# Kernel optimization log

Hardware: AMD Instinct MI355X
Metric: run time of the kernel (lower is better)

Reference implementation:

```python
import jax, jax.numpy as jnp
import numpy as np

N_HEADS = 4
NS_STEPS = 5
NS_EPS = 1e-7

def newtonschulz5(G):
    # G: [out, in]; quintic Newton-Schulz, 5 steps. out==in here so no transpose branch needed,
    # but keep the static-shape check for faithfulness.
    a, b, c = 3.4445, -4.775, 2.0315
    X = G / (jnp.linalg.norm(G) + NS_EPS)
    transposed = G.shape[0] > G.shape[1]
    if transposed:
        X = X.T
    def step(X, _):
        A = X @ X.T
        B = b * A + c * (A @ A)
        return a * X + B @ X, None
    X, _ = jax.lax.scan(step, X, None, length=NS_STEPS)
    if transposed:
        X = X.T
    return X

def setup_inputs() -> dict:
    key = jax.random.key(0)
    k1, k2, k3, k4, k5 = jax.random.split(key, 5)
    B, S, D_in, D_out, r = 4, 2048, 4096, 4096, 16
    init_std = 0.01 / np.sqrt(D_out * r)
    return {
        "x": jax.random.normal(k1, (B, S, D_in), dtype=jnp.float32),
        "W": jax.random.normal(k2, (D_out, D_in), dtype=jnp.float32) * 0.02,
        "bias": jax.random.normal(k3, (D_out,), dtype=jnp.float32) * 0.02,
        "lora_A": jax.random.normal(k4, (r, D_in), dtype=jnp.float32),
        "lora_B": jax.random.normal(k5, (D_out, r), dtype=jnp.float32) * init_std,
    }

def reference(x, W, bias, lora_A, lora_B):
    # base linear (frozen weights); dropout is identity (p=0 / eval)
    base_out = jnp.einsum('bsi,oi->bso', x, W) + bias
    r, D_in = lora_A.shape
    D_out = lora_B.shape[0]
    hr = r // N_HEADS
    Ah = lora_A.reshape(N_HEADS, hr, D_in)                       # [h, hr, in]
    Bh = lora_B.reshape(D_out, N_HEADS, hr).transpose(1, 0, 2)    # [h, out, hr]
    G = jnp.einsum('hor,hri->hoi', Bh, Ah)                        # [h, out, in]
    alpha = jnp.sqrt(jnp.sum(G * G, axis=(1, 2)))                 # per-head Frobenius norm
    M = jax.vmap(newtonschulz5)(G)                                # [h, out, in]
    lora_out = jnp.einsum('h,hoi,bsi->bso', alpha, M, x)
    return base_out + lora_out
```

## Files before the change

kernel.cpp:

```cpp
#include <hip/hip_runtime.h>
#include <math.h>

#define MDIM 8192
#define NDIM 4096
#define KDIM 4096

typedef __attribute__((ext_vector_type(8))) _Float16 h8;
typedef __attribute__((ext_vector_type(4))) _Float16 h4;
typedef __attribute__((ext_vector_type(4))) float f32x4;

typedef const __attribute__((address_space(1))) void* gas_ptr;
typedef __attribute__((address_space(3))) void* las_ptr;

__device__ inline void load16_to_lds(const void* g, void* l) {
  __builtin_amdgcn_global_load_lds((gas_ptr)g, (las_ptr)l, 16, 0, 0);
}

__device__ inline void mm4(const double* A, const double* B, double* C) {
#pragma unroll
  for (int p = 0; p < 4; ++p)
#pragma unroll
    for (int q = 0; q < 4; ++q) {
      double s = 0.0;
#pragma unroll
      for (int r = 0; r < 4; ++r) s += A[p * 4 + r] * B[r * 4 + q];
      C[p * 4 + q] = s;
    }
}
__device__ inline void mm4_bt(const double* A, const double* B, double* C) {
#pragma unroll
  for (int p = 0; p < 4; ++p)
#pragma unroll
    for (int q = 0; q < 4; ++q) {
      double s = 0.0;
#pragma unroll
      for (int r = 0; r < 4; ++r) s += A[p * 4 + r] * B[q * 4 + r];
      C[p * 4 + q] = s;
    }
}

__global__ void ns_kernel(const float* __restrict__ lora_A,
                          const float* __restrict__ lora_B,
                          float* __restrict__ E) {
  const int h = blockIdx.x;
  const int tid = threadIdx.x;
  const int lane = tid & 63;
  const int wave = tid >> 6;

  float gu[16], gv[16];
#pragma unroll
  for (int e = 0; e < 16; ++e) { gu[e] = 0.f; gv[e] = 0.f; }

  for (int o = tid; o < NDIM; o += 256) {
    const float4 bv = *(const float4*)(lora_B + (size_t)o * 16 + h * 4);
    const float bb[4] = {bv.x, bv.y, bv.z, bv.w};
#pragma unroll
    for (int p = 0; p < 4; ++p)
#pragma unroll
      for (int q = 0; q < 4; ++q) gu[p * 4 + q] += bb[p] * bb[q];
  }
  for (int i = tid; i < KDIM; i += 256) {
    float aa[4];
#pragma unroll
    for (int p = 0; p < 4; ++p) aa[p] = lora_A[(size_t)(h * 4 + p) * KDIM + i];
#pragma unroll
    for (int p = 0; p < 4; ++p)
#pragma unroll
      for (int q = 0; q < 4; ++q) gv[p * 4 + q] += aa[p] * aa[q];
  }

#pragma unroll
  for (int e = 0; e < 16; ++e) {
#pragma unroll
    for (int off = 32; off > 0; off >>= 1) {
      gu[e] += __shfl_down(gu[e], off, 64);
      gv[e] += __shfl_down(gv[e], off, 64);
    }
  }
  __shared__ float pu[4][16], pv[4][16];
  if (lane == 0) {
#pragma unroll
    for (int e = 0; e < 16; ++e) { pu[wave][e] = gu[e]; pv[wave][e] = gv[e]; }
  }
  __syncthreads();

  if (tid == 0) {
    double gud[16], gvd[16];
#pragma unroll
    for (int e = 0; e < 16; ++e) {
      gud[e] = (double)pu[0][e] + pu[1][e] + pu[2][e] + pu[3][e];
      gvd[e] = (double)pv[0][e] + pv[1][e] + pv[2][e] + pv[3][e];
    }
    double tr = 0.0;
#pragma unroll
    for (int e = 0; e < 16; ++e) tr += gud[e] * gvd[e];
    const double alpha = sqrt(tr);
    const double n0 = alpha + 1e-7;

    double C[16] = {0};
    C[0] = C[5] = C[10] = C[15] = 1.0 / n0;

    const double a = 3.4445, b = -4.775, c = 2.0315;
    for (int it = 0; it < 5; ++it) {
      double T1[16], D[16], DG[16], DGD[16], GuC[16], F[16], Cn[16];
      mm4(C, gvd, T1);
      mm4_bt(T1, C, D);
      mm4(D, gud, DG);
      mm4(DG, D, DGD);
      mm4(gud, C, GuC);
#pragma unroll
      for (int e = 0; e < 16; ++e) F[e] = b * D[e] + c * DGD[e];
      mm4(F, GuC, Cn);
#pragma unroll
      for (int e = 0; e < 16; ++e) C[e] = a * C[e] + Cn[e];
    }
#pragma unroll
    for (int e = 0; e < 16; ++e) E[h * 16 + e] = (float)(alpha * C[e]);
  }
}

__global__ void prep_kernel(const float* __restrict__ x,
                            const float* __restrict__ W,
                            const float* __restrict__ lora_A,
                            const float* __restrict__ lora_B,
                            const float* __restrict__ E,
                            _Float16* __restrict__ Wh,
                            _Float16* __restrict__ Xh) {
  const int tid = threadIdx.x;
  if (blockIdx.x < NDIM) {
    const int o = blockIdx.x;
    __shared__ float coef[16];
    if (tid < 16) {
      const int h = tid >> 2, q = tid & 3;
      float s = 0.f;
#pragma unroll
      for (int p = 0; p < 4; ++p)
        s += lora_B[(size_t)o * 16 + h * 4 + p] * E[h * 16 + p * 4 + q];
      coef[tid] = s;
    }
    __syncthreads();
    float cf[16];
#pragma unroll
    for (int k = 0; k < 16; ++k) cf[k] = coef[k];

    for (int i = tid * 4; i < KDIM; i += 1024) {
      float4 acc = *(const float4*)(W + (size_t)o * KDIM + i);
#pragma unroll
      for (int k = 0; k < 16; ++k) {
        const float4 av = *(const float4*)(lora_A + (size_t)k * KDIM + i);
        acc.x += cf[k] * av.x; acc.y += cf[k] * av.y;
        acc.z += cf[k] * av.z; acc.w += cf[k] * av.w;
      }
      h4 pk;
      pk[0] = (_Float16)acc.x; pk[1] = (_Float16)acc.y;
      pk[2] = (_Float16)acc.z; pk[3] = (_Float16)acc.w;
      *(h4*)(Wh + (size_t)o * KDIM + i) = pk;
    }
  } else {
    const size_t t = (size_t)(blockIdx.x - NDIM) * 256 + tid;
    const size_t base = t * 8;
    const float4 a = *(const float4*)(x + base);
    const float4 b = *(const float4*)(x + base + 4);
    h8 o;
    o[0] = (_Float16)a.x; o[1] = (_Float16)a.y; o[2] = (_Float16)a.z; o[3] = (_Float16)a.w;
    o[4] = (_Float16)b.x; o[5] = (_Float16)b.y; o[6] = (_Float16)b.z; o[7] = (_Float16)b.w;
    *(h8*)(Xh + base) = o;
  }
}

__launch_bounds__(256, 2)
__global__ void gemm_kernel(const _Float16* __restrict__ Xh,
                            const _Float16* __restrict__ Wh,
                            const float* __restrict__ bias,
                            float* __restrict__ out) {
  __shared__ __align__(16) _Float16 As[128 * 32];
  __shared__ __align__(16) _Float16 Bs[128 * 32];

  const int tid = threadIdx.x;
  const int bn = blockIdx.x;
  const int bm = blockIdx.y;
  const int lane = tid & 63;
  const int wave = tid >> 6;
  const int wm = (wave >> 1) * 64;
  const int wn = (wave & 1) * 64;
  const int quad = lane >> 4;
  const int r16 = lane & 15;

  const int c0 = tid;
  const int c1 = tid + 256;
  const int row0 = c0 >> 2, row1 = c1 >> 2;
  const int col0 = ((c0 & 3) ^ ((row0 >> 1) & 3)) * 8;
  const int col1 = ((c1 & 3) ^ ((row1 >> 1) & 3)) * 8;
  const size_t Ar0 = (size_t)(bm * 128 + row0) * KDIM + col0;
  const size_t Ar1 = (size_t)(bm * 128 + row1) * KDIM + col1;
  const size_t Br0 = (size_t)(bn * 128 + row0) * KDIM + col0;
  const size_t Br1 = (size_t)(bn * 128 + row1) * KDIM + col1;
  const int ldsb = tid * 16;

  f32x4 acc[4][4] = {};

  for (int k0 = 0; k0 < KDIM; k0 += 32) {
    __syncthreads();
    load16_to_lds(Xh + Ar0 + k0, (char*)As + ldsb);
    load16_to_lds(Xh + Ar1 + k0, (char*)As + ldsb + 4096);
    load16_to_lds(Wh + Br0 + k0, (char*)Bs + ldsb);
    load16_to_lds(Wh + Br1 + k0, (char*)Bs + ldsb + 4096);
    __syncthreads();

    h8 a[4], b[4];
#pragma unroll
    for (int i = 0; i < 4; ++i) {
      const int ra = wm + i * 16 + r16;
      const int rb = wn + i * 16 + r16;
      a[i] = *(const h8*)(As + ra * 32 + ((quad ^ ((ra >> 1) & 3)) * 8));
      b[i] = *(const h8*)(Bs + rb * 32 + ((quad ^ ((rb >> 1) & 3)) * 8));
    }
#pragma unroll
    for (int i = 0; i < 4; ++i)
#pragma unroll
      for (int j = 0; j < 4; ++j)
        acc[i][j] = __builtin_amdgcn_mfma_f32_16x16x32_f16(a[i], b[j], acc[i][j], 0, 0, 0);
  }

  const int orow = bm * 128 + wm + quad * 4;
  const int ocol = bn * 128 + wn + r16;
#pragma unroll
  for (int j = 0; j < 4; ++j) {
    const int cc = ocol + j * 16;
    const float bv = bias[cc];
#pragma unroll
    for (int i = 0; i < 4; ++i) {
#pragma unroll
      for (int rg = 0; rg < 4; ++rg) {
        const int rr = orow + i * 16 + rg;
        out[(size_t)rr * NDIM + cc] = acc[i][j][rg] + bv;
      }
    }
  }
}

extern "C" void kernel_launch(void* const* d_in, const int* in_sizes, int n_in,
                              void* d_out, int out_size, void* d_ws, size_t ws_size,
                              hipStream_t stream) {
  const float* x      = (const float*)d_in[0];
  const float* W      = (const float*)d_in[1];
  const float* bias   = (const float*)d_in[2];
  const float* lora_A = (const float*)d_in[3];
  const float* lora_B = (const float*)d_in[4];
  float* out = (float*)d_out;

  char* ws = (char*)d_ws;
  float* E = (float*)ws;
  _Float16* Wh = (_Float16*)(ws + 1024);
  _Float16* Xh = (_Float16*)(ws + 1024 + (size_t)NDIM * KDIM * 2);

  ns_kernel<<<dim3(4), dim3(256), 0, stream>>>(lora_A, lora_B, E);
  prep_kernel<<<dim3(NDIM + (MDIM * KDIM) / (256 * 8)), dim3(256), 0, stream>>>(
      x, W, lora_A, lora_B, E, Wh, Xh);
  gemm_kernel<<<dim3(NDIM / 128, MDIM / 128), dim3(256), 0, stream>>>(Xh, Wh, bias, out);
}
```

Before: 655.2 us.

## Rewrite GEMM as 256x256 tile, 8-wave, double-buffered pipelined kernel

```diff
diff --git a/kernel.cpp b/kernel.cpp
--- a/kernel.cpp
+++ b/kernel.cpp
@@ -168,75 +168,129 @@
   }
 }
 
-__launch_bounds__(256, 2)
+__launch_bounds__(512, 2)
 __global__ void gemm_kernel(const _Float16* __restrict__ Xh,
                             const _Float16* __restrict__ Wh,
                             const float* __restrict__ bias,
                             float* __restrict__ out) {
-  __shared__ __align__(16) _Float16 As[128 * 32];
-  __shared__ __align__(16) _Float16 Bs[128 * 32];
+  __shared__ __align__(16) _Float16 sA0h0[128 * 64], sA0h1[128 * 64];
+  __shared__ __align__(16) _Float16 sA1h0[128 * 64], sA1h1[128 * 64];
+  __shared__ __align__(16) _Float16 sB0h0[128 * 64], sB0h1[128 * 64];
+  __shared__ __align__(16) _Float16 sB1h0[128 * 64], sB1h1[128 * 64];
 
   const int tid = threadIdx.x;
-  const int bn = blockIdx.x;
-  const int bm = blockIdx.y;
   const int lane = tid & 63;
   const int wave = tid >> 6;
-  const int wm = (wave >> 1) * 64;
-  const int wn = (wave & 1) * 64;
+  const int wm = wave >> 2;
+  const int wn = wave & 3;
   const int quad = lane >> 4;
   const int r16 = lane & 15;
-
-  const int c0 = tid;
-  const int c1 = tid + 256;
-  const int row0 = c0 >> 2, row1 = c1 >> 2;
-  const int col0 = ((c0 & 3) ^ ((row0 >> 1) & 3)) * 8;
-  const int col1 = ((c1 & 3) ^ ((row1 >> 1) & 3)) * 8;
-  const size_t Ar0 = (size_t)(bm * 128 + row0) * KDIM + col0;
-  const size_t Ar1 = (size_t)(bm * 128 + row1) * KDIM + col1;
-  const size_t Br0 = (size_t)(bn * 128 + row0) * KDIM + col0;
-  const size_t Br1 = (size_t)(bn * 128 + row1) * KDIM + col1;
+  const int sw = r16 & 7;
+
+  const int lin = blockIdx.x;
+  const int wg = (lin & 7) * 64 + (lin >> 3);
+  const int bm = wg >> 4;
+  const int bn = wg & 15;
+
+  const int row0 = tid >> 3;
+  const int lc0 = (tid & 7) ^ (row0 & 7);
+  const size_t off0 = (size_t)row0 * KDIM + lc0 * 8;
   const int ldsb = tid * 16;
-
-  f32x4 acc[4][4] = {};
-
-  for (int k0 = 0; k0 < KDIM; k0 += 32) {
-    __syncthreads();
-    load16_to_lds(Xh + Ar0 + k0, (char*)As + ldsb);
-    load16_to_lds(Xh + Ar1 + k0, (char*)As + ldsb + 4096);
-    load16_to_lds(Wh + Br0 + k0, (char*)Bs + ldsb);
-    load16_to_lds(Wh + Br1 + k0, (char*)Bs + ldsb + 4096);
-    __syncthreads();
-
-    h8 a[4], b[4];
-#pragma unroll
-    for (int i = 0; i < 4; ++i) {
-      const int ra = wm + i * 16 + r16;
-      const int rb = wn + i * 16 + r16;
-      a[i] = *(const h8*)(As + ra * 32 + ((quad ^ ((ra >> 1) & 3)) * 8));
-      b[i] = *(const h8*)(Bs + rb * 32 + ((quad ^ ((rb >> 1) & 3)) * 8));
-    }
-#pragma unroll
-    for (int i = 0; i < 4; ++i)
-#pragma unroll
-      for (int j = 0; j < 4; ++j)
-        acc[i][j] = __builtin_amdgcn_mfma_f32_16x16x32_f16(a[i], b[j], acc[i][j], 0, 0, 0);
-  }
-
-  const int orow = bm * 128 + wm + quad * 4;
-  const int ocol = bn * 128 + wn + r16;
-#pragma unroll
-  for (int j = 0; j < 4; ++j) {
-    const int cc = ocol + j * 16;
-    const float bv = bias[cc];
-#pragma unroll
-    for (int i = 0; i < 4; ++i) {
-#pragma unroll
-      for (int rg = 0; rg < 4; ++rg) {
-        const int rr = orow + i * 16 + rg;
-        out[(size_t)rr * NDIM + cc] = acc[i][j][rg] + bv;
-      }
-    }
-  }
+  const _Float16* pA0 = Xh + (size_t)(bm * 256) * KDIM;
+  const _Float16* pA1 = pA0 + (size_t)128 * KDIM;
+  const _Float16* pB0 = Wh + (size_t)(bn * 256) * KDIM;
+  const _Float16* pB1 = pB0 + (size_t)128 * KDIM;
+
+  const int aRow = (wm * 64 + r16) * 64;
+  const int bRow = (wn * 32 + r16) * 64;
+  const int c0 = (quad ^ sw) * 8;
+  const int c1 = ((quad + 4) ^ sw) * 8;
+
+  f32x4 acc[2][2][4][2] = {};
+
+#define STAGE(arr, p, koff) do {                                               \
+    load16_to_lds((p) + off0 + (koff), (char*)(arr) + ldsb);                   \
+    load16_to_lds((p) + off0 + (size_t)64 * KDIM + (koff),                     \
+                  (char*)(arr) + ldsb + 8192);                                 \
+  } while (0)
+
+#define FENCE() asm volatile("" ::: "memory")
+#define BAR() do { FENCE(); __builtin_amdgcn_s_barrier(); FENCE(); } while (0)
+#define VM4() asm volatile("s_waitcnt vmcnt(4)" ::: "memory")
+#define VM0() asm volatile("s_waitcnt vmcnt(0)" ::: "memory")
+
+#define PHASE(Aarr, Barr, mq, nq, STMT, WCNT) do {                             \
+    h8 av[4][2], bv[2][2];                                                     \
+    _Pragma("unroll")                                                          \
+    for (int f = 0; f < 4; ++f) {                                              \
+      av[f][0] = *(const h8*)&Aarr[aRow + f * 1024 + c0];                      \
+      av[f][1] = *(const h8*)&Aarr[aRow + f * 1024 + c1];                      \
+    }                                                                          \
+    _Pragma("unroll")                                                          \
+    for (int g = 0; g < 2; ++g) {                                              \
+      bv[g][0] = *(const h8*)&Barr[bRow + g * 1024 + c0];                      \
+      bv[g][1] = *(const h8*)&Barr[bRow + g * 1024 + c1];                      \
+    }                                                                          \
+    STMT;                                                                      \
+    BAR();                                                                     \
+    __builtin_amdgcn_s_setprio(1);                                             \
+    _Pragma("unroll")                                                          \
+    for (int f = 0; f < 4; ++f)                                                \
+      _Pragma("unroll")                                                        \
+      for (int g = 0; g < 2; ++g) {                                            \
+        acc[mq][nq][f][g] = __builtin_amdgcn_mfma_f32_16x16x32_f16(            \
+            av[f][0], bv[g][0], acc[mq][nq][f][g], 0, 0, 0);                   \
+        acc[mq][nq][f][g] = __builtin_amdgcn_mfma_f32_16x16x32_f16(            \
+            av[f][1], bv[g][1], acc[mq][nq][f][g], 0, 0, 0);                   \
+      }                                                                        \
+    __builtin_amdgcn_s_setprio(0);                                             \
+    WCNT;                                                                      \
+    BAR();                                                                     \
+  } while (0)
+
+#define TILE(t, cA0, cA1, cB0, cB1, oA1, oB1) do {                             \
+    PHASE(cA0, cB0, 0, 0,                                                      \
+          { if ((t) + 1 < NT) STAGE(oA1, pA1, ((t) + 1) * 64); }, ;);          \
+    PHASE(cA0, cB1, 0, 1,                                                      \
+          { if ((t) + 1 < NT) STAGE(oB1, pB1, ((t) + 1) * 64); }, ;);          \
+    PHASE(cA1, cB0, 1, 0,                                                      \
+          { if ((t) + 2 < NT) STAGE(cA0, pA0, ((t) + 2) * 64); }, ;);          \
+    PHASE(cA1, cB1, 1, 1,                                                      \
+          { if ((t) + 2 < NT) STAGE(cB0, pB0, ((t) + 2) * 64); },              \
+          { if ((t) + 2 < NT) VM4(); else VM0(); });                           \
+  } while (0)
+
+  constexpr int NT = KDIM / 64;
+
+  STAGE(sA0h0, pA0, 0);  STAGE(sB0h0, pB0, 0);
+  STAGE(sA0h1, pA1, 0);  STAGE(sB0h1, pB1, 0);
+  STAGE(sA1h0, pA0, 64); STAGE(sB1h0, pB0, 64);
+  VM4();
+  BAR();
+
+#pragma unroll 1
+  for (int t2 = 0; t2 < NT; t2 += 2) {
+    TILE(t2,     sA0h0, sA0h1, sB0h0, sB0h1, sA1h1, sB1h1);
+    TILE(t2 + 1, sA1h0, sA1h1, sB1h0, sB1h1, sA0h1, sB0h1);
+  }
+
+#pragma unroll
+  for (int mq = 0; mq < 2; ++mq)
+#pragma unroll
+    for (int f = 0; f < 4; ++f) {
+      float* po = out + (size_t)(bm * 256 + mq * 128 + wm * 64 + f * 16 + quad * 4) * NDIM;
+#pragma unroll
+      for (int nq = 0; nq < 2; ++nq)
+#pragma unroll
+        for (int g = 0; g < 2; ++g) {
+          const int ocol = bn * 256 + nq * 128 + wn * 32 + g * 16 + r16;
+          const float bb = bias[ocol];
+          const f32x4 v = acc[mq][nq][f][g];
+#pragma unroll
+          for (int rg = 0; rg < 4; ++rg)
+            po[(size_t)rg * NDIM + ocol] = v[rg] + bb;
+        }
+    }
 }
 
 extern "C" void kernel_launch(void* const* d_in, const int* in_sizes, int n_in,
@@ -257,5 +311,5 @@
   ns_kernel<<<dim3(4), dim3(256), 0, stream>>>(lora_A, lora_B, E);
   prep_kernel<<<dim3(NDIM + (MDIM * KDIM) / (256 * 8)), dim3(256), 0, stream>>>(
       x, W, lora_A, lora_B, E, Wh, Xh);
-  gemm_kernel<<<dim3(NDIM / 128, MDIM / 128), dim3(256), 0, stream>>>(Xh, Wh, bias, out);
-}
+  gemm_kernel<<<dim3(512), dim3(512), 0, stream>>>(Xh, Wh, bias, out);
+}
```

Result: faster. 604.5 us (-7.7%).
